# Performance work log

Hardware: AMD Instinct MI355X
Metric: run time of the kernel (lower is better)

## Reference

```python
import jax, jax.numpy as jnp
import numpy as np

N_NODES = 100000
N_EDGES = 1600000
GENE_DIM = 256
HID = 128
NUM_CLASSES = 2
BN_EPS = 1e-5


def setup_inputs() -> dict:
    key = jax.random.key(0)
    ks = jax.random.split(key, 24)
    g = lambda k, shape, scale: (jax.random.normal(k, shape, dtype=jnp.float32) * scale)
    inp = {
        "x": g(ks[0], (N_NODES, GENE_DIM), 1.0),
        "edge_index": jax.random.randint(ks[1], (2, N_EDGES), 0, N_NODES, dtype=jnp.int64),
        # GCNConv weights (glorot-ish scale) and biases
        "W1": g(ks[2], (GENE_DIM, HID), 1.0 / np.sqrt(GENE_DIM)), "b1": jnp.zeros((HID,), jnp.float32),
        "W2": g(ks[3], (HID, 2 * HID), 1.0 / np.sqrt(HID)), "b2": jnp.zeros((2 * HID,), jnp.float32),
        "W3": g(ks[4], (2 * HID, HID), 1.0 / np.sqrt(2 * HID)), "b3": jnp.zeros((HID,), jnp.float32),
        "W4": g(ks[5], (HID, HID // 2), 1.0 / np.sqrt(HID)), "b4": jnp.zeros((HID // 2,), jnp.float32),
        "Wc": g(ks[6], (HID // 2, NUM_CLASSES), 1.0 / np.sqrt(HID // 2)), "bc": jnp.zeros((NUM_CLASSES,), jnp.float32),
        # BatchNorm affine params
        "g1": jnp.ones((HID,), jnp.float32), "be1": jnp.zeros((HID,), jnp.float32),
        "g2": jnp.ones((2 * HID,), jnp.float32), "be2": jnp.zeros((2 * HID,), jnp.float32),
        "g3": jnp.ones((HID,), jnp.float32), "be3": jnp.zeros((HID,), jnp.float32),
        "g4": jnp.ones((HID // 2,), jnp.float32), "be4": jnp.zeros((HID // 2,), jnp.float32),
    }
    return inp


def _batchnorm(h, gamma, beta):
    # training-mode BatchNorm1d: per-feature batch stats (biased variance)
    mean = h.mean(axis=0)
    var = ((h - mean) ** 2).mean(axis=0)
    return gamma * (h - mean) * jax.lax.rsqrt(var + BN_EPS) + beta


def _gcn_conv(h, W, b, src, dst, norm, n):
    # PyG GCNConv: linear transform, then sym-normalized aggregation over
    # edges (self-loops already included in src/dst/norm), then bias.
    m = h @ W                                   # [n, d_out]
    msg = m[src] * norm[:, None]                # [E+n, d_out] gather
    agg = jax.ops.segment_sum(msg, dst, num_segments=n)  # scatter-add
    return agg + b


def reference(x, edge_index, W1, b1, W2, b2, W3, b3, W4, b4, Wc, bc,
              g1, be1, g2, be2, g3, be3, g4, be4):
    n = x.shape[0]
    loop = jnp.arange(n, dtype=edge_index.dtype)
    src = jnp.concatenate([edge_index[0], loop])  # add self-loops
    dst = jnp.concatenate([edge_index[1], loop])
    deg = jax.ops.segment_sum(jnp.ones_like(dst, dtype=x.dtype), dst, num_segments=n)
    dinv = jax.lax.rsqrt(jnp.maximum(deg, 1.0))
    norm = dinv[src] * dinv[dst]                  # D^-1/2 (A+I) D^-1/2

    h = jax.nn.relu(_gcn_conv(x, W1, b1, src, dst, norm, n))
    h = _batchnorm(h, g1, be1)
    h = jax.nn.relu(_gcn_conv(h, W2, b2, src, dst, norm, n))
    h = _batchnorm(h, g2, be2)
    h = jax.nn.relu(_gcn_conv(h, W3, b3, src, dst, norm, n))
    h = _batchnorm(h, g3, be3)
    out4 = jax.nn.relu(_gcn_conv(h, W4, b4, src, dst, norm, n))
    bn4 = _batchnorm(out4, g4, be4)
    logits = bn4 @ Wc + bc
    return (logits, out4, bn4)
```

## Files before the change

kernel.cpp:

```cpp
#include <hip/hip_runtime.h>
#include <hip/hip_bf16.h>

#define N_NODES 100000
#define N_EDGES 1600000
#define NB ((N_NODES + 255) / 256)
#define CHUNK 16384
#define NBLK ((N_EDGES + CHUNK - 1) / CHUNK)
#define NSHADOW 64

typedef short sh8 __attribute__((ext_vector_type(8)));
typedef float f32x4 __attribute__((ext_vector_type(4)));

__device__ __forceinline__ float bf2f(unsigned short s) {
    return __uint_as_float(((unsigned int)s) << 16);
}
__device__ __forceinline__ unsigned short f2bf(float f) {
    unsigned int u = __float_as_uint(f);
    unsigned int r = (u + 0x7FFFu + ((u >> 16) & 1u)) >> 16;
    return (unsigned short)r;
}
__device__ __forceinline__ float blo(unsigned int u) { return __uint_as_float(u << 16); }
__device__ __forceinline__ float bhi(unsigned int u) { return __uint_as_float(u & 0xffff0000u); }


__global__ __launch_bounds__(256) void k_hist(const int* __restrict__ ei, int* __restrict__ histG) {
    __shared__ int hist[NB];
    int blk = blockIdx.x, t = threadIdx.x;
    for (int b = t; b < NB; b += 256) hist[b] = 0;
    __syncthreads();
    int e0 = blk * CHUNK;
    int e1 = min(e0 + CHUNK, N_EDGES);
    for (int e = e0 + t; e < e1; e += 256) atomicAdd(&hist[ei[N_EDGES + e] >> 8], 1);
    __syncthreads();
    for (int b = t; b < NB; b += 256) histG[b * NBLK + blk] = hist[b];
}

__global__ __launch_bounds__(128) void k_scanrow(int* __restrict__ histG, int* __restrict__ rowsum) {
    __shared__ int sm[128];
    int b = blockIdx.x, t = threadIdx.x;
    int v = (t < NBLK) ? histG[b * NBLK + t] : 0;
    sm[t] = v; __syncthreads();
    for (int d = 1; d < 128; d <<= 1) {
        int add = (t >= d) ? sm[t - d] : 0;
        __syncthreads(); sm[t] += add; __syncthreads();
    }
    if (t < NBLK) histG[b * NBLK + t] = sm[t] - v;
    if (t == 127) rowsum[b] = sm[127];
}

__global__ __launch_bounds__(512) void k_scanbkt(const int* __restrict__ rowsum, int* __restrict__ rowbase) {
    __shared__ int sm[512];
    int t = threadIdx.x;
    int v = (t < NB) ? rowsum[t] : 0;
    sm[t] = v; __syncthreads();
    for (int d = 1; d < 512; d <<= 1) {
        int add = (t >= d) ? sm[t - d] : 0;
        __syncthreads(); sm[t] += add; __syncthreads();
    }
    if (t <= NB) rowbase[t] = sm[t] - v;
}

__global__ __launch_bounds__(256) void k_part(const int* __restrict__ ei, const int* __restrict__ histG,
                                              const int* __restrict__ rowbase, unsigned* __restrict__ pairs) {
    __shared__ int cur[NB];
    int blk = blockIdx.x, t = threadIdx.x;
    for (int b = t; b < NB; b += 256) cur[b] = rowbase[b] + histG[b * NBLK + blk];
    __syncthreads();
    int e0 = blk * CHUNK;
    int e1 = min(e0 + CHUNK, N_EDGES);
    for (int e = e0 + t; e < e1; e += 256) {
        int s = ei[e], d = ei[N_EDGES + e];
        int pos = atomicAdd(&cur[d >> 8], 1);
        pairs[pos] = ((unsigned)s << 8) | (unsigned)(d & 255);
    }
}

__global__ __launch_bounds__(256) void k_bsort(const unsigned* __restrict__ pairs, const int* __restrict__ rowbase,
                                               int* __restrict__ col, int* __restrict__ basep,
                                               int* __restrict__ deg, float* __restrict__ dinv,
                                               float* __restrict__ sdeg) {
    __shared__ int cnt[256];
    __shared__ int sm[256];
    __shared__ int cur[256];
    int b = blockIdx.x, t = threadIdx.x;
    int base = rowbase[b], end = rowbase[b + 1];
    cnt[t] = 0; __syncthreads();
    for (int e = base + t; e < end; e += 256) atomicAdd(&cnt[pairs[e] & 255], 1);
    __syncthreads();
    int v = cnt[t];
    sm[t] = v; __syncthreads();
    for (int d = 1; d < 256; d <<= 1) {
        int add = (t >= d) ? sm[t - d] : 0;
        __syncthreads(); sm[t] += add; __syncthreads();
    }
    int excl = sm[t] - v;
    cur[t] = excl;
    int gd = (b << 8) + t;
    if (gd < N_NODES) {
        basep[gd] = base + excl;
        deg[gd] = v;
        dinv[gd] = rsqrtf((float)(v + 1));
        sdeg[gd] = sqrtf((float)(v + 1));
    }
    __syncthreads();
    for (int e = base + t; e < end; e += 256) {
        unsigned p = pairs[e];
        int pos = atomicAdd(&cur[p & 255], 1);
        col[base + pos] = (int)(p >> 8);
    }
}

__global__ __launch_bounds__(256) void k_svec(const int* __restrict__ col, const int* __restrict__ basep,
                                              const int* __restrict__ deg, const float* __restrict__ dinv,
                                              float* __restrict__ svec) {
    int w = (blockIdx.x * 256 + threadIdx.x) >> 6;
    if (w >= N_NODES) return;
    int lane = threadIdx.x & 63;
    int start = basep[w], cnt = deg[w];
    float s = 0.f;
    for (int j = lane; j < cnt; j += 64) s += dinv[col[start + j]];
#pragma unroll
    for (int off = 32; off; off >>= 1) s += __shfl_down(s, off, 64);
    if (lane == 0) { float di = dinv[w]; svec[w] = di * (s + di); }
}


__global__ void k_wconv_all(const float* __restrict__ W1, const float* __restrict__ W2,
                            const float* __restrict__ W3, const float* __restrict__ W4,
                            unsigned short* __restrict__ Wt1, unsigned short* __restrict__ Wt2,
                            unsigned short* __restrict__ Wt3, unsigned short* __restrict__ Wt4) {
    int idx = blockIdx.x * 256 + threadIdx.x;
    const float* W; unsigned short* Wt; int K, N, base;
    if (idx < 32768)       { W = W1; Wt = Wt1; K = 256; N = 128; base = 0; }
    else if (idx < 65536)  { W = W2; Wt = Wt2; K = 128; N = 256; base = 32768; }
    else if (idx < 98304)  { W = W3; Wt = Wt3; K = 256; N = 128; base = 65536; }
    else if (idx < 106496) { W = W4; Wt = Wt4; K = 128; N = 64;  base = 98304; }
    else return;
    int li = idx - base;
    int n = li / K, k = li - n * K;
    Wt[li] = f2bf(W[(size_t)k * N + n]);
}


__global__ __launch_bounds__(256) void k_bnred(float* __restrict__ shadow, float* __restrict__ dst) {
    int f = blockIdx.x * 256 + threadIdx.x;
    float s = 0.f;
#pragma unroll
    for (int i = 0; i < NSHADOW; ++i) {
        s += shadow[i * 512 + f];
        shadow[i * 512 + f] = 0.f;
    }
    dst[f] = s;
}


template <int D, bool INF32, bool RESCALE>
__global__ __launch_bounds__(256) void k_bnstats(const void* __restrict__ h,
                                                 const float* __restrict__ sdeg,
                                                 float* __restrict__ shadow) {
    constexpr int VEC = INF32 ? 4 : 8;
    constexpr int TPR = D / VEC;
    constexpr int RPB = 256 / TPR;
    const int tid = threadIdx.x;
    const int rg = tid / TPR;
    const int oc = tid % TPR;
    const int fb = oc * VEC;

    float s1[VEC], s2[VEC];
#pragma unroll
    for (int k = 0; k < VEC; ++k) { s1[k] = 0.f; s2[k] = 0.f; }

    for (int r = blockIdx.x * RPB + rg; r < N_NODES; r += gridDim.x * RPB) {
        float rs = 1.f;
        if constexpr (RESCALE) rs = sdeg[r];
        if constexpr (INF32) {
            float4 v = *(const float4*)((const float*)h + (size_t)r * D + fb);
            float vv[4] = {v.x, v.y, v.z, v.w};
#pragma unroll
            for (int k = 0; k < 4; ++k) {
                float val = vv[k];
                if constexpr (RESCALE) val *= rs;
                s1[k] += val; s2[k] += val * val;
            }
        } else {
            uint4 u = *(const uint4*)((const unsigned short*)h + (size_t)r * D + fb);
            unsigned uu[4] = {u.x, u.y, u.z, u.w};
#pragma unroll
            for (int k = 0; k < 4; ++k) {
                float v0 = blo(uu[k]), v1 = bhi(uu[k]);
                if constexpr (RESCALE) { v0 *= rs; v1 *= rs; }
                s1[2 * k] += v0;     s2[2 * k] += v0 * v0;
                s1[2 * k + 1] += v1; s2[2 * k + 1] += v1 * v1;
            }
        }
    }

    __shared__ float red[2][D];
    for (int i = tid; i < 2 * D; i += 256) ((float*)red)[i] = 0.f;
    __syncthreads();
#pragma unroll
    for (int k = 0; k < VEC; ++k) {
        atomicAdd(&red[0][fb + k], s1[k]);
        atomicAdd(&red[1][fb + k], s2[k]);
    }
    __syncthreads();
    float* slot = shadow + ((blockIdx.x & (NSHADOW - 1)) << 9);
    for (int i = tid; i < 2 * D; i += 256) {
        int f = (i < D) ? i : (256 + i - D);
        float v = (i < D) ? red[0][i] : red[1][i - D];
        atomicAdd(&slot[f], v);
    }
}


template <int BN, int AMODE, bool BIASRELU, bool DSCALE>
__global__ __launch_bounds__(512) void k_gemm3(const void* __restrict__ Ain,
                                               const unsigned short* __restrict__ Wt,
                                               const float* __restrict__ sums_in,
                                               const float* __restrict__ gamma,
                                               const float* __restrict__ beta,
                                               const float* __restrict__ svec,
                                               const float* __restrict__ bias,
                                               const float* __restrict__ dinv,
                                               unsigned short* __restrict__ Mout,
                                               int K, int NTOT) {
    constexpr int BK = 64;
    constexpr int LDA = 72;
    constexpr int MF = 2;
    constexpr int NF = BN / 64;
    constexpr int BP = BN / 64;
    __shared__ unsigned short As[64 * LDA];
    __shared__ unsigned short Bs[BN * LDA];
    __shared__ float ss_sc[256];
    __shared__ float ss_sh[256];
    const int tid = threadIdx.x;
    const int lane = tid & 63;
    const int wv = tid >> 6;
    const int wm = wv >> 2;
    const int wn = wv & 3;
    const int row0 = blockIdx.x * 64;
    const int col0 = blockIdx.y * BN;

    if constexpr (AMODE >= 1) {
        for (int f = tid; f < K; f += 512) {
            float mean = sums_in[f] * (1.f / N_NODES);
            float var = sums_in[256 + f] * (1.f / N_NODES) - mean * mean;
            float inv = rsqrtf(var + 1e-5f);
            float sc = gamma[f] * inv;
            ss_sc[f] = sc;
            ss_sh[f] = beta[f] - mean * sc;
        }
        __syncthreads();
    }

    const int sr = tid >> 3;
    const int scc = (tid & 7) * 8;

    float4 fa[2];
    uint4 ua;
    uint4 ub[BP];
    float sv = 0.f;

    auto LOAD = [&](int k0) {
        int gr = row0 + sr;
        if constexpr (AMODE == 0) {
            const float* Af = (const float*)Ain;
            fa[0] = make_float4(0.f, 0.f, 0.f, 0.f); fa[1] = fa[0];
            if (gr < N_NODES) {
                const float* p0 = Af + (size_t)gr * K + k0 + scc;
                fa[0] = *(const float4*)p0;
                fa[1] = *(const float4*)(p0 + 4);
            }
        } else {
            const unsigned short* Ab = (const unsigned short*)Ain;
            ua = make_uint4(0, 0, 0, 0);
            if (gr < N_NODES) ua = *(const uint4*)(Ab + (size_t)gr * K + k0 + scc);
            if constexpr (AMODE == 2) sv = (gr < N_NODES) ? svec[gr] : 0.f;
        }
#pragma unroll
        for (int p = 0; p < BP; ++p)
            ub[p] = *(const uint4*)(Wt + (size_t)(col0 + p * 64 + sr) * K + k0 + scc);
    };

    auto WRITE = [&](int k0) {
        alignas(16) unsigned short tmp[8];
        if constexpr (AMODE == 0) {
            tmp[0] = f2bf(fa[0].x); tmp[1] = f2bf(fa[0].y);
            tmp[2] = f2bf(fa[0].z); tmp[3] = f2bf(fa[0].w);
            tmp[4] = f2bf(fa[1].x); tmp[5] = f2bf(fa[1].y);
            tmp[6] = f2bf(fa[1].z); tmp[7] = f2bf(fa[1].w);
        } else {
            const unsigned short* pr = (const unsigned short*)&ua;
#pragma unroll
            for (int q = 0; q < 8; ++q) {
                float sc = ss_sc[k0 + scc + q];
                float sh = ss_sh[k0 + scc + q];
                float val;
                if constexpr (AMODE == 2) val = bf2f(pr[q]) * sc + sh * sv;
                else val = bf2f(pr[q]) * sc + sh;
                tmp[q] = f2bf(val);
            }
        }
        *(uint4*)&As[sr * LDA + scc] = *(const uint4*)tmp;
#pragma unroll
        for (int p = 0; p < BP; ++p) *(uint4*)&Bs[(p * 64 + sr) * LDA + scc] = ub[p];
    };

    f32x4 acc[MF][NF];
#pragma unroll
    for (int i = 0; i < MF; ++i)
#pragma unroll
        for (int j = 0; j < NF; ++j)
#pragma unroll
            for (int r = 0; r < 4; ++r) acc[i][j][r] = 0.f;

    LOAD(0);
    WRITE(0);
    __syncthreads();
    const int nk = K / BK;
    for (int kt = 1; kt <= nk; ++kt) {
        if (kt < nk) LOAD(kt * BK);
#pragma unroll
        for (int ks = 0; ks < 2; ++ks) {
            sh8 af[MF], bfr[NF];
#pragma unroll
            for (int i = 0; i < MF; ++i)
                af[i] = *(const sh8*)&As[(wm * 32 + i * 16 + (lane & 15)) * LDA + ks * 32 + (lane >> 4) * 8];
#pragma unroll
            for (int j = 0; j < NF; ++j)
                bfr[j] = *(const sh8*)&Bs[(wn * NF * 16 + j * 16 + (lane & 15)) * LDA + ks * 32 + (lane >> 4) * 8];
#pragma unroll
            for (int i = 0; i < MF; ++i)
#pragma unroll
                for (int j = 0; j < NF; ++j)
                    acc[i][j] = __builtin_amdgcn_mfma_f32_16x16x32_bf16(af[i], bfr[j], acc[i][j], 0, 0, 0);
        }
        __syncthreads();
        if (kt < nk) {
            WRITE(kt * BK);
            __syncthreads();
        }
    }

#pragma unroll
    for (int i = 0; i < MF; ++i) {
#pragma unroll
        for (int r = 0; r < 4; ++r) {
            int grow = row0 + wm * 32 + i * 16 + (lane >> 4) * 4 + r;
            if (grow >= N_NODES) continue;
            float rsc = 1.f;
            if constexpr (DSCALE) rsc = dinv[grow];
#pragma unroll
            for (int j = 0; j < NF; ++j) {
                int gcol = col0 + wn * NF * 16 + j * 16 + (lane & 15);
                float v = acc[i][j][r];
                if constexpr (BIASRELU) v = fmaxf(v + bias[gcol], 0.f);
                if constexpr (DSCALE) v *= rsc;
                Mout[(size_t)grow * NTOT + gcol] = f2bf(v);
            }
        }
    }
}


template <int D, bool PRE, bool OUTF32, bool OUTSCALE>
__global__ __launch_bounds__(256) void k_agg(const unsigned short* __restrict__ m,
                                             const int* __restrict__ col,
                                             const int* __restrict__ basep,
                                             const int* __restrict__ deg,
                                             const float* __restrict__ dinv,
                                             const float* __restrict__ bias,
                                             void* __restrict__ out) {
    constexpr int VPL = D / 64;
    constexpr int BT = 16;
    const int w = (blockIdx.x * 256 + threadIdx.x) >> 6;
    if (w >= N_NODES) return;
    const int lane = threadIdx.x & 63;
    const int fo = lane * VPL;
    const unsigned short* mfo = m + fo;
    float acc[VPL];
#pragma unroll
    for (int k = 0; k < VPL; ++k) acc[k] = 0.f;

    const int start = basep[w];
    const int cnt = deg[w];
    const int total = cnt + 1;

    for (int j = 0; j < total; j += BT) {
        int sx[BT];
#pragma unroll
        for (int i = 0; i < BT; ++i) {
            int idx = j + i;
            int ca = start + idx;
            ca = (ca < N_EDGES) ? ca : (N_EDGES - 1);
            int c = col[ca];
            sx[i] = (idx < cnt) ? c : w;
        }
        if constexpr (VPL == 2) {
            unsigned u[BT];
#pragma unroll
            for (int i = 0; i < BT; ++i) u[i] = *(const unsigned*)(mfo + (size_t)sx[i] * D);
#pragma unroll
            for (int i = 0; i < BT; ++i) {
                if (j + i < total) { acc[0] += blo(u[i]); acc[1] += bhi(u[i]); }
            }
        } else {
            unsigned short us[BT];
#pragma unroll
            for (int i = 0; i < BT; ++i) us[i] = mfo[(size_t)sx[i] * D];
#pragma unroll
            for (int i = 0; i < BT; ++i) {
                if (j + i < total) acc[0] += bf2f(us[i]);
            }
        }
    }

    float di = dinv[w];
    float o[VPL];
    if constexpr (PRE) {
#pragma unroll
        for (int k = 0; k < VPL; ++k) o[k] = acc[k] * di;
    } else {
#pragma unroll
        for (int k = 0; k < VPL; ++k) {
            o[k] = fmaxf(acc[k] * di + bias[fo + k], 0.f);
            if constexpr (OUTSCALE) o[k] *= di;
        }
    }

    if constexpr (OUTF32) {
        float* of = (float*)out;
#pragma unroll
        for (int k = 0; k < VPL; ++k) of[(size_t)w * D + fo + k] = o[k];
    } else {
        unsigned short* ob = (unsigned short*)out + (size_t)w * D + fo;
        if constexpr (VPL == 2) {
            unsigned int u = (unsigned)f2bf(o[0]) | ((unsigned)f2bf(o[1]) << 16);
            *(unsigned int*)ob = u;
        } else {
            ob[0] = f2bf(o[0]);
        }
    }
}


__global__ __launch_bounds__(256) void k_bnlog(const float* __restrict__ out4, const float* __restrict__ sums,
                                               const float* __restrict__ gamma, const float* __restrict__ beta,
                                               const float* __restrict__ Wc, const float* __restrict__ bc,
                                               float* __restrict__ bn4, float* __restrict__ logits) {
    int gw = (blockIdx.x * 256 + threadIdx.x) >> 6;
    if (gw >= N_NODES) return;
    int f = threadIdx.x & 63;
    float mean = sums[f] * (1.f / N_NODES);
    float var = sums[256 + f] * (1.f / N_NODES) - mean * mean;
    float inv = rsqrtf(var + 1e-5f);
    float sc = gamma[f] * inv;
    float sh = beta[f] - mean * sc;
    float v = out4[(size_t)gw * 64 + f];
    float bn = v * sc + sh;
    bn4[(size_t)gw * 64 + f] = bn;
    float a0 = bn * Wc[2 * f];
    float a1 = bn * Wc[2 * f + 1];
#pragma unroll
    for (int off = 32; off; off >>= 1) {
        a0 += __shfl_down(a0, off, 64);
        a1 += __shfl_down(a1, off, 64);
    }
    if (f == 0) {
        logits[2 * gw] = a0 + bc[0];
        logits[2 * gw + 1] = a1 + bc[1];
    }
}


extern "C" void kernel_launch(void* const* d_in, const int* in_sizes, int n_in,
                              void* d_out, int out_size, void* d_ws, size_t ws_size,
                              hipStream_t stream) {
    const float* x  = (const float*)d_in[0];
    const int* ei   = (const int*)d_in[1];
    const float* W1 = (const float*)d_in[2];  const float* b1  = (const float*)d_in[3];
    const float* W2 = (const float*)d_in[4];  const float* b2  = (const float*)d_in[5];
    const float* W3 = (const float*)d_in[6];  const float* b3  = (const float*)d_in[7];
    const float* W4 = (const float*)d_in[8];  const float* b4  = (const float*)d_in[9];
    const float* Wc = (const float*)d_in[10]; const float* bc  = (const float*)d_in[11];
    const float* g1 = (const float*)d_in[12]; const float* be1 = (const float*)d_in[13];
    const float* g2 = (const float*)d_in[14]; const float* be2 = (const float*)d_in[15];
    const float* g3 = (const float*)d_in[16]; const float* be3 = (const float*)d_in[17];
    const float* g4 = (const float*)d_in[18]; const float* be4 = (const float*)d_in[19];

    char* wsb = (char*)d_ws;
    size_t off = 0;
    auto alloc = [&](size_t bytes) -> void* {
        void* p = wsb + off;
        off = (off + bytes + 511) & ~(size_t)511;
        return p;
    };
    int* deg     = (int*)alloc((size_t)N_NODES * 4);
    int* basep   = (int*)alloc((size_t)N_NODES * 4);
    float* dinv  = (float*)alloc((size_t)N_NODES * 4);
    float* sdeg  = (float*)alloc((size_t)N_NODES * 4);
    float* svec  = (float*)alloc((size_t)N_NODES * 4);
    int* col     = (int*)alloc((size_t)N_EDGES * 4);
    unsigned* pairs = (unsigned*)alloc((size_t)N_EDGES * 4);
    int* histG   = (int*)alloc((size_t)NB * NBLK * 4);
    int* rowsum  = (int*)alloc((size_t)NB * 4);
    int* rowbase = (int*)alloc((size_t)(NB + 1) * 4);
    float* sums  = (float*)alloc(2048 * 4);
    float* shadow = (float*)alloc((size_t)NSHADOW * 512 * 4);
    unsigned short* Wt1 = (unsigned short*)alloc((size_t)256 * 128 * 2);
    unsigned short* Wt2 = (unsigned short*)alloc((size_t)128 * 256 * 2);
    unsigned short* Wt3 = (unsigned short*)alloc((size_t)256 * 128 * 2);
    unsigned short* Wt4 = (unsigned short*)alloc((size_t)128 * 64 * 2);
    unsigned short* mb = (unsigned short*)alloc((size_t)N_NODES * 128 * 2);
    unsigned short* hb = (unsigned short*)alloc((size_t)N_NODES * 256 * 2);

    float* sums1 = sums, *sums2 = sums + 512, *sums3 = sums + 1024, *sums4 = sums + 1536;

    float* outLogits = (float*)d_out;
    float* out4 = outLogits + (size_t)N_NODES * 2;
    float* bn4  = out4 + (size_t)N_NODES * 64;

    hipMemsetAsync(sums, 0, 2048 * 4, stream);
    hipMemsetAsync(shadow, 0, (size_t)NSHADOW * 512 * 4, stream);

    k_hist<<<NBLK, 256, 0, stream>>>(ei, histG);
    k_scanrow<<<NB, 128, 0, stream>>>(histG, rowsum);
    k_scanbkt<<<1, 512, 0, stream>>>(rowsum, rowbase);
    k_part<<<NBLK, 256, 0, stream>>>(ei, histG, rowbase, pairs);
    k_bsort<<<NB, 256, 0, stream>>>(pairs, rowbase, col, basep, deg, dinv, sdeg);
    k_svec<<<(N_NODES + 3) / 4, 256, 0, stream>>>(col, basep, deg, dinv, svec);

    k_wconv_all<<<(106496 + 255) / 256, 256, 0, stream>>>(W1, W2, W3, W4, Wt1, Wt2, Wt3, Wt4);

    const int GBM = (N_NODES + 63) / 64;
    const int AB = (N_NODES + 3) / 4;
    const int SB = 512;

    k_gemm3<128, 0, false, true><<<dim3(GBM, 1), 512, 0, stream>>>(
        x, Wt1, nullptr, nullptr, nullptr, nullptr, nullptr, dinv, mb, 256, 128);
    k_agg<128, false, false, true><<<AB, 256, 0, stream>>>(
        mb, col, basep, deg, dinv, b1, hb);
    k_bnstats<128, false, true><<<SB, 256, 0, stream>>>(hb, sdeg, shadow);
    k_bnred<<<2, 256, 0, stream>>>(shadow, sums1);

    k_agg<128, true, false, false><<<AB, 256, 0, stream>>>(
        hb, col, basep, deg, dinv, nullptr, mb);
    k_gemm3<128, 2, true, false><<<dim3(GBM, 2), 512, 0, stream>>>(
        mb, Wt2, sums1, g1, be1, svec, b2, nullptr, hb, 128, 256);
    k_bnstats<256, false, false><<<SB, 256, 0, stream>>>(hb, nullptr, shadow);
    k_bnred<<<2, 256, 0, stream>>>(shadow, sums2);

    k_gemm3<128, 1, false, true><<<dim3(GBM, 1), 512, 0, stream>>>(
        hb, Wt3, sums2, g2, be2, nullptr, nullptr, dinv, mb, 256, 128);
    k_agg<128, false, false, false><<<AB, 256, 0, stream>>>(
        mb, col, basep, deg, dinv, b3, hb);
    k_bnstats<128, false, false><<<SB, 256, 0, stream>>>(hb, nullptr, shadow);
    k_bnred<<<2, 256, 0, stream>>>(shadow, sums3);

    k_gemm3<64, 1, false, true><<<dim3(GBM, 1), 512, 0, stream>>>(
        hb, Wt4, sums3, g3, be3, nullptr, nullptr, dinv, mb, 128, 64);
    k_agg<64, false, true, false><<<AB, 256, 0, stream>>>(
        mb, col, basep, deg, dinv, b4, out4);
    k_bnstats<64, true, false><<<SB, 256, 0, stream>>>(out4, nullptr, shadow);
    k_bnred<<<2, 256, 0, stream>>>(shadow, sums4);
    k_bnlog<<<(N_NODES * 64 + 255) / 256, 256, 0, stream>>>(out4, sums4, g4, be4, Wc, bc, bn4, outLogits);
}
```

Baseline: 653.1 us.

## Split neighbor list across half-waves in aggregation and widen per-lane vector loads

The aggregation kernel now has each wave split a node's edge list between two 32-lane halves. Each lane gathers 2 or 4 bf16 features with wider loads, and the halves combine their partial sums with a cross-half shuffle. The padded fixed 16-wide batch with per-element bounds checks is replaced by an 8-wide unrolled main loop plus a scalar tail, and the self-loop is handled separately. The goal is more memory-level parallelism per gather and fewer wasted loads for low-degree nodes. In exchange, each node gets fewer outstanding loads per half, and the extra tail and shuffle code adds overhead.

```diff
diff --git a/kernel.cpp b/kernel.cpp
--- a/kernel.cpp
+++ b/kernel.cpp
@@ -371,12 +371,13 @@
                                              const float* __restrict__ dinv,
                                              const float* __restrict__ bias,
                                              void* __restrict__ out) {
-    constexpr int VPL = D / 64;
-    constexpr int BT = 16;
+    constexpr int VPL = D / 32;
     const int w = (blockIdx.x * 256 + threadIdx.x) >> 6;
     if (w >= N_NODES) return;
     const int lane = threadIdx.x & 63;
-    const int fo = lane * VPL;
+    const int half = lane >> 5;
+    const int hl = lane & 31;
+    const int fo = hl * VPL;
     const unsigned short* mfo = m + fo;
     float acc[VPL];
 #pragma unroll
@@ -384,36 +385,57 @@
 
     const int start = basep[w];
     const int cnt = deg[w];
-    const int total = cnt + 1;
-
-    for (int j = 0; j < total; j += BT) {
-        int sx[BT];
-#pragma unroll
-        for (int i = 0; i < BT; ++i) {
-            int idx = j + i;
-            int ca = start + idx;
-            ca = (ca < N_EDGES) ? ca : (N_EDGES - 1);
-            int c = col[ca];
-            sx[i] = (idx < cnt) ? c : w;
-        }
-        if constexpr (VPL == 2) {
-            unsigned u[BT];
-#pragma unroll
-            for (int i = 0; i < BT; ++i) u[i] = *(const unsigned*)(mfo + (size_t)sx[i] * D);
-#pragma unroll
-            for (int i = 0; i < BT; ++i) {
-                if (j + i < total) { acc[0] += blo(u[i]); acc[1] += bhi(u[i]); }
+    const int c0 = cnt >> 1;
+    const int jb = half ? c0 : 0;
+    const int je = half ? cnt : c0;
+
+    int j = jb;
+    for (; j + 8 <= je; j += 8) {
+        int sx[8];
+#pragma unroll
+        for (int i = 0; i < 8; ++i) sx[i] = col[start + j + i];
+        if constexpr (VPL == 4) {
+            uint2 u[8];
+#pragma unroll
+            for (int i = 0; i < 8; ++i) u[i] = *(const uint2*)(mfo + (size_t)sx[i] * D);
+#pragma unroll
+            for (int i = 0; i < 8; ++i) {
+                acc[0] += blo(u[i].x); acc[1] += bhi(u[i].x);
+                acc[2] += blo(u[i].y); acc[3] += bhi(u[i].y);
             }
         } else {
-            unsigned short us[BT];
-#pragma unroll
-            for (int i = 0; i < BT; ++i) us[i] = mfo[(size_t)sx[i] * D];
-#pragma unroll
-            for (int i = 0; i < BT; ++i) {
-                if (j + i < total) acc[0] += bf2f(us[i]);
-            }
-        }
-    }
+            unsigned u[8];
+#pragma unroll
+            for (int i = 0; i < 8; ++i) u[i] = *(const unsigned*)(mfo + (size_t)sx[i] * D);
+#pragma unroll
+            for (int i = 0; i < 8; ++i) { acc[0] += blo(u[i]); acc[1] += bhi(u[i]); }
+        }
+    }
+    for (; j < je; ++j) {
+        int s0 = col[start + j];
+        if constexpr (VPL == 4) {
+            uint2 u0 = *(const uint2*)(mfo + (size_t)s0 * D);
+            acc[0] += blo(u0.x); acc[1] += bhi(u0.x);
+            acc[2] += blo(u0.y); acc[3] += bhi(u0.y);
+        } else {
+            unsigned u0 = *(const unsigned*)(mfo + (size_t)s0 * D);
+            acc[0] += blo(u0); acc[1] += bhi(u0);
+        }
+    }
+    if (half == 0) {
+        if constexpr (VPL == 4) {
+            uint2 u0 = *(const uint2*)(mfo + (size_t)w * D);
+            acc[0] += blo(u0.x); acc[1] += bhi(u0.x);
+            acc[2] += blo(u0.y); acc[3] += bhi(u0.y);
+        } else {
+            unsigned u0 = *(const unsigned*)(mfo + (size_t)w * D);
+            acc[0] += blo(u0); acc[1] += bhi(u0);
+        }
+    }
+#pragma unroll
+    for (int k = 0; k < VPL; ++k) acc[k] += __shfl_xor(acc[k], 32, 64);
+
+    if (half != 0) return;
 
     float di = dinv[w];
     float o[VPL];
@@ -429,16 +451,22 @@
     }
 
     if constexpr (OUTF32) {
-        float* of = (float*)out;
-#pragma unroll
-        for (int k = 0; k < VPL; ++k) of[(size_t)w * D + fo + k] = o[k];
+        float* of = (float*)out + (size_t)w * D + fo;
+        if constexpr (VPL == 4) {
+            *(float4*)of = make_float4(o[0], o[1], o[2], o[3]);
+        } else {
+            *(float2*)of = make_float2(o[0], o[1]);
+        }
     } else {
         unsigned short* ob = (unsigned short*)out + (size_t)w * D + fo;
-        if constexpr (VPL == 2) {
+        if constexpr (VPL == 4) {
+            uint2 u;
+            u.x = (unsigned)f2bf(o[0]) | ((unsigned)f2bf(o[1]) << 16);
+            u.y = (unsigned)f2bf(o[2]) | ((unsigned)f2bf(o[3]) << 16);
+            *(uint2*)ob = u;
+        } else {
             unsigned int u = (unsigned)f2bf(o[0]) | ((unsigned)f2bf(o[1]) << 16);
             *(unsigned int*)ob = u;
-        } else {
-            ob[0] = f2bf(o[0]);
         }
     }
 }
```

After: 659.2 us. Within noise of the previous version (+0.9%).
